# Kernel tuning notes

Hardware: AMD Instinct MI355X
Metric: run time of the kernel (lower is better)

Reference implementation:

```python
import jax, jax.numpy as jnp
import numpy as np

D_MODEL, D_STATE, D_CONV, D_INNER = 768, 16, 4, 1536
B, L = 4, 4096


def setup_inputs() -> dict:
    key = jax.random.key(0)
    ks = jax.random.split(key, 9)
    s = 0.02
    return {
        "x": jax.random.normal(ks[0], (B, L, D_MODEL), jnp.float32),
        "w_in": jax.random.normal(ks[1], (2 * D_INNER, D_MODEL), jnp.float32) * s,
        "w_conv": jax.random.normal(ks[2], (D_INNER, 1, D_CONV), jnp.float32) * 0.2,
        "w_xproj": jax.random.normal(ks[3], (2 * D_STATE + 1, D_INNER), jnp.float32) * s,
        "w_dt": jax.random.normal(ks[4], (D_INNER, 1), jnp.float32) * s,
        "b_dt": jax.random.normal(ks[5], (D_INNER,), jnp.float32) * 0.1,
        "a_log": jnp.log(jnp.tile(jnp.arange(1, D_STATE + 1, dtype=jnp.float32), (D_INNER, 1))),
        "d_param": jnp.ones((D_INNER,), jnp.float32),
        "w_out": jax.random.normal(ks[6], (D_MODEL, D_INNER), jnp.float32) * s,
    }


def _mamba_fwd(x, w_in, w_conv, w_xproj, w_dt, b_dt, a_log, d_param, w_out):
    Lseq = x.shape[1]
    xz = x @ w_in.T                                  # [B,L,2*Di]
    xs, z = jnp.split(xz, 2, axis=-1)                # [B,L,Di] each
    # depthwise causal conv1d (padding=d_conv-1, then crop to L == left-pad causal)
    xc = xs.transpose(0, 2, 1)                       # [B,Di,L]
    xc = jax.lax.conv_general_dilated(
        xc, w_conv, window_strides=(1,), padding=[(D_CONV - 1, 0)],
        feature_group_count=D_INNER, dimension_numbers=("NCH", "OIH", "NCH"))
    xs = jax.nn.silu(xc.transpose(0, 2, 1))          # [B,L,Di]
    # selective SSM parameters
    proj = xs @ w_xproj.T                            # [B,L,1+2N]
    delta_raw = proj[..., :1]                        # [B,L,1]
    b_proj = proj[..., 1:1 + D_STATE]                # [B,L,N]
    c_proj = proj[..., 1 + D_STATE:]                 # [B,L,N]
    delta = jax.nn.softplus(delta_raw @ w_dt.T + b_dt)   # [B,L,Di]
    a_mat = -jnp.exp(a_log)                          # [Di,N]

    def step(h, inp):
        dt, bt, ct, xt = inp                         # [B,Di],[B,N],[B,N],[B,Di]
        a_bar = jnp.exp(dt[:, :, None] * a_mat)      # [B,Di,N]
        h = a_bar * h + dt[:, :, None] * bt[:, None, :] * xt[:, :, None]
        y = jnp.einsum("bn,bdn->bd", ct, h) + d_param * xt
        return h, y

    h0 = jnp.zeros((x.shape[0], D_INNER, D_STATE), x.dtype)
    # time-major inputs for scan
    inputs = (delta.transpose(1, 0, 2), b_proj.transpose(1, 0, 2),
              c_proj.transpose(1, 0, 2), xs.transpose(1, 0, 2))
    _, ys = jax.lax.scan(step, h0, inputs, length=Lseq)
    y = ys.transpose(1, 0, 2)                        # [B,L,Di]
    return (y * jax.nn.silu(z)) @ w_out.T            # [B,L,d_model]


def reference(x, w_in, w_conv, w_xproj, w_dt, b_dt, a_log, d_param, w_out):
    return _mamba_fwd(x, w_in, w_conv, w_xproj, w_dt, b_dt, a_log, d_param, w_out)
```

## Files before the change

### kernel.cpp

```cpp
#include <hip/hip_runtime.h>
#include <hip/hip_bf16.h>

#define D_MODEL 768
#define D_STATE 16
#define D_INNER 1536
#define BB 4
#define LL 4096

typedef __bf16 bf16_t;
typedef __bf16 bf16x8 __attribute__((ext_vector_type(8)));
typedef __bf16 bf16x4 __attribute__((ext_vector_type(4)));
typedef float f32x4 __attribute__((ext_vector_type(4)));

__global__ __launch_bounds__(256) void cvt_all(
    const float4* __restrict__ x4, bf16x4* __restrict__ xb4,
    const float* __restrict__ w_in, const float* __restrict__ w_out,
    const float* __restrict__ w_xproj, bf16_t* __restrict__ wibf,
    bf16_t* __restrict__ wobf, bf16_t* __restrict__ wxpbf) {
  int i = blockIdx.x * 256 + threadIdx.x;
  float4 v = x4[i];
  bf16x4 o;
  o[0] = (bf16_t)v.x; o[1] = (bf16_t)v.y; o[2] = (bf16_t)v.z; o[3] = (bf16_t)v.w;
  xb4[i] = o;
  if (i < 1179648) {
    wibf[i] = (bf16_t)w_in[i];
    wibf[i + 1179648] = (bf16_t)w_in[i + 1179648];
    wobf[i] = (bf16_t)w_out[i];
    if (i < 196608) {
      int row = i / 1536;
      wxpbf[i] = (row < 33) ? (bf16_t)w_xproj[i] : (bf16_t)0.f;
    }
  }
}

template <typename CT, bool ATOMIC, bool GATE>
__global__ __launch_bounds__(256, 4) void gemm_bf16_mfma(
    const bf16_t* __restrict__ A, const bf16_t* __restrict__ B,
    CT* __restrict__ C, int K, int Klen, int ldc, int ncols) {
  __shared__ __align__(16) bf16_t As[128 * 32];
  __shared__ __align__(16) bf16_t Bs[128 * 32];
  const int t = threadIdx.x;
  const int lane = t & 63;
  const int wid = t >> 6;
  const int wm = (wid >> 1) * 64;
  const int wn = (wid & 1) * 64;
  const long Nbase = (long)blockIdx.x * 128;
  const long Mbase = (long)blockIdx.y * 128;
  const long koff = (long)blockIdx.z * Klen;

  const int r0 = t >> 2;
  const int c0 = (((t & 3) ^ ((t >> 2) & 3))) * 8;

  const bf16_t* ap0 = A + (Mbase + r0) * K + koff + c0;
  const bf16_t* ap1 = ap0 + 64 * (long)K;
  const bf16_t* bp0 = B + (Nbase + r0) * K + koff + c0;
  const bf16_t* bp1 = bp0 + 64 * (long)K;

  f32x4 acc[4][4];
#pragma unroll
  for (int i = 0; i < 4; ++i)
#pragma unroll
    for (int j = 0; j < 4; ++j) acc[i][j] = (f32x4){0.f, 0.f, 0.f, 0.f};

  const int lrow = lane & 15;
  const int lchunk = ((lane >> 4) ^ (lrow & 3)) * 8;

  for (int k0 = 0; k0 < Klen; k0 += 32) {
    if (k0) __syncthreads();
    __builtin_amdgcn_global_load_lds(
        (const __attribute__((address_space(1))) unsigned int*)ap0,
        (__attribute__((address_space(3))) unsigned int*)(&As[t * 8]), 16, 0, 0);
    __builtin_amdgcn_global_load_lds(
        (const __attribute__((address_space(1))) unsigned int*)ap1,
        (__attribute__((address_space(3))) unsigned int*)(&As[(256 + t) * 8]), 16, 0, 0);
    __builtin_amdgcn_global_load_lds(
        (const __attribute__((address_space(1))) unsigned int*)bp0,
        (__attribute__((address_space(3))) unsigned int*)(&Bs[t * 8]), 16, 0, 0);
    __builtin_amdgcn_global_load_lds(
        (const __attribute__((address_space(1))) unsigned int*)bp1,
        (__attribute__((address_space(3))) unsigned int*)(&Bs[(256 + t) * 8]), 16, 0, 0);
    ap0 += 32; ap1 += 32; bp0 += 32; bp1 += 32;
    __syncthreads();

    bf16x8 af[4], bfr[4];
#pragma unroll
    for (int i = 0; i < 4; ++i)
      af[i] = *(const bf16x8*)(&As[(wm + i * 16 + lrow) * 32 + lchunk]);
#pragma unroll
    for (int j = 0; j < 4; ++j)
      bfr[j] = *(const bf16x8*)(&Bs[(wn + j * 16 + lrow) * 32 + lchunk]);
#pragma unroll
    for (int i = 0; i < 4; ++i)
#pragma unroll
      for (int j = 0; j < 4; ++j)
        acc[i][j] = __builtin_amdgcn_mfma_f32_16x16x32_bf16(af[i], bfr[j], acc[i][j], 0, 0, 0);
  }

  const int orow = (lane >> 4) * 4;
  const int ocol = lane & 15;
#pragma unroll
  for (int i = 0; i < 4; ++i) {
#pragma unroll
    for (int j = 0; j < 4; ++j) {
      int col = (int)Nbase + wn + j * 16 + ocol;
      if (col < ncols) {
        long rowb = Mbase + wm + i * 16 + orow;
#pragma unroll
        for (int r = 0; r < 4; ++r) {
          float v = acc[i][j][r];
          if (ATOMIC) {
            atomicAdd((float*)&C[(rowb + r) * (long)ldc + col], v);
          } else {
            if (GATE && col >= 1536) v = v / (1.f + __expf(-v));
            C[(rowb + r) * (long)ldc + col] = (CT)v;
          }
        }
      }
    }
  }
}

__global__ __launch_bounds__(256) void conv_silu(const bf16_t* __restrict__ xz,
                                                 const float4* __restrict__ wconv,
                                                 bf16_t* __restrict__ xc) {
  long T = (long)blockIdx.x * 256 + threadIdx.x;
  int d = (int)(T % 1536);
  long r = T / 1536;
  int l0 = (int)(r & 511) * 8;
  long b = r >> 9;
  float4 w = wconv[d];
  const bf16_t* xs = xz + ((long)b * LL + l0) * 3072 + d;
  float v[11];
  if (l0 == 0) {
    v[0] = 0.f; v[1] = 0.f; v[2] = 0.f;
  } else {
    v[0] = (float)xs[-3 * 3072]; v[1] = (float)xs[-2 * 3072]; v[2] = (float)xs[-3072];
  }
#pragma unroll
  for (int j = 3; j < 11; ++j) v[j] = (float)xs[(j - 3) * 3072];
  bf16_t* o = xc + ((long)b * LL + l0) * 1536 + d;
#pragma unroll
  for (int i = 0; i < 8; ++i) {
    float acc = w.x * v[i];
    acc = fmaf(w.y, v[i + 1], acc);
    acc = fmaf(w.z, v[i + 2], acc);
    acc = fmaf(w.w, v[i + 3], acc);
    o[(long)i * 1536] = (bf16_t)(acc / (1.f + __expf(-acc)));
  }
}

__device__ __forceinline__ float softplus_f(float x) {
  return (x > 15.f) ? x : __logf(1.f + __expf(x));
}


__global__ __launch_bounds__(256) void scan_p1(
    const bf16_t* __restrict__ xc, const float* __restrict__ proj,
    const float* __restrict__ w_dt, const float* __restrict__ b_dt,
    float4* __restrict__ hend, float* __restrict__ Ssum) {
  __shared__ __align__(16) float prs_bc[64 * 32];
  __shared__ float prs_d[64];
  const int c = blockIdx.x;
  const int b = blockIdx.z;
  const int t = threadIdx.x;
  const int d = blockIdx.y * 256 + t;
  const long blbase = (long)b * LL + (long)c * 64;

  const float* src = proj + blbase * 33;
  for (int i = t; i < 2112; i += 256) {
    int row = i / 33, col = i - row * 33;
    float v = src[i];
    if (col == 0) prs_d[row] = v; else prs_bc[row * 32 + col - 1] = v;
  }
  __syncthreads();

  const float wdt = w_dt[d];
  const float bdt = b_dt[d];
  float h[16];
#pragma unroll
  for (int n = 0; n < 16; ++n) h[n] = 0.f;
  float S = 0.f;

  for (int l = 0; l < 64; ++l) {
    float delta = softplus_f(fmaf(prs_d[l], wdt, bdt));
    S += delta;
    float E = __expf(-delta);
    float xt = (float)xc[(blbase + l) * 1536 + d];
    float dx = delta * xt;
    const f32x4* bc = (const f32x4*)&prs_bc[l * 32];
    float ab = E;
#pragma unroll
    for (int q = 0; q < 4; ++q) {
      f32x4 Bq = bc[q];
#pragma unroll
      for (int k = 0; k < 4; ++k) {
        h[q * 4 + k] = fmaf(ab, h[q * 4 + k], dx * Bq[k]);
        ab *= E;
      }
    }
  }
  long ob = ((long)b * 64 + c) * 1536 + d;
#pragma unroll
  for (int q = 0; q < 4; ++q)
    hend[ob * 4 + q] = (float4){h[q * 4], h[q * 4 + 1], h[q * 4 + 2], h[q * 4 + 3]};
  Ssum[ob] = S;
}

__global__ __launch_bounds__(256) void scan_p2(float* __restrict__ hend,
                                               const float* __restrict__ Ssum,
                                               const float* __restrict__ a_log) {
  int idx = blockIdx.x * 256 + threadIdx.x;
  int n = idx & 15;
  int dn = idx >> 4;
  int d = dn % 1536;
  int b = dn / 1536;
  float a = -__expf(a_log[d * 16 + n]);
  float hs = 0.f;
  for (int c = 0; c < 64; ++c) {
    long ob = ((long)b * 64 + c) * 1536 + d;
    float e = hend[ob * 16 + n];
    float S = Ssum[ob];
    hend[ob * 16 + n] = hs;
    hs = fmaf(__expf(a * S), hs, e);
  }
}

__global__ __launch_bounds__(256) void scan_p3(
    const bf16_t* __restrict__ xc, const float* __restrict__ proj,
    const bf16_t* __restrict__ xz, const float* __restrict__ w_dt,
    const float* __restrict__ b_dt, const float* __restrict__ d_param,
    const float4* __restrict__ hstart, bf16_t* __restrict__ ymul) {
  __shared__ __align__(16) float prs_bc[64 * 32];
  __shared__ float prs_d[64];
  const int c = blockIdx.x;
  const int b = blockIdx.z;
  const int t = threadIdx.x;
  const int d = blockIdx.y * 256 + t;
  const long blbase = (long)b * LL + (long)c * 64;

  const float* src = proj + blbase * 33;
  for (int i = t; i < 2112; i += 256) {
    int row = i / 33, col = i - row * 33;
    float v = src[i];
    if (col == 0) prs_d[row] = v; else prs_bc[row * 32 + col - 1] = v;
  }
  __syncthreads();

  const float wdt = w_dt[d];
  const float bdt = b_dt[d];
  const float Dv = d_param[d];
  long ob = ((long)b * 64 + c) * 1536 + d;
  float h[16];
#pragma unroll
  for (int q = 0; q < 4; ++q) {
    float4 h4 = hstart[ob * 4 + q];
    h[q * 4] = h4.x; h[q * 4 + 1] = h4.y; h[q * 4 + 2] = h4.z; h[q * 4 + 3] = h4.w;
  }

  for (int l = 0; l < 64; ++l) {
    float delta = softplus_f(fmaf(prs_d[l], wdt, bdt));
    float E = __expf(-delta);
    float xt = (float)xc[(blbase + l) * 1536 + d];
    float dx = delta * xt;
    const f32x4* bc = (const f32x4*)&prs_bc[l * 32];
    float ab = E;
    float y = 0.f;
#pragma unroll
    for (int q = 0; q < 4; ++q) {
      f32x4 Bq = bc[q];
      f32x4 Cq = bc[q + 4];
#pragma unroll
      for (int k = 0; k < 4; ++k) {
        h[q * 4 + k] = fmaf(ab, h[q * 4 + k], dx * Bq[k]);
        y = fmaf(Cq[k], h[q * 4 + k], y);
        ab *= E;
      }
    }
    y = fmaf(Dv, xt, y);
    float gz = (float)xz[(blbase + l) * 3072 + 1536 + d];
    ymul[(blbase + l) * 1536 + d] = (bf16_t)(y * gz);
  }
}

extern "C" void kernel_launch(void* const* d_in, const int* in_sizes, int n_in,
                              void* d_out, int out_size, void* d_ws, size_t ws_size,
                              hipStream_t stream) {
  const float* x       = (const float*)d_in[0];
  const float* w_in    = (const float*)d_in[1];
  const float* w_conv  = (const float*)d_in[2];
  const float* w_xproj = (const float*)d_in[3];
  const float* w_dt    = (const float*)d_in[4];
  const float* b_dt    = (const float*)d_in[5];
  const float* a_log   = (const float*)d_in[6];
  const float* d_param = (const float*)d_in[7];
  const float* w_out   = (const float*)d_in[8];
  float* out = (float*)d_out;

  char* ws = (char*)d_ws;
  bf16_t* xz    = (bf16_t*)ws;  ws += 100663296;
  bf16_t* xc    = (bf16_t*)ws;  ws += 50331648;
  float*  proj  = (float*)ws;   ws += 2162688;
  float*  hend  = (float*)ws;   ws += 25165824;
  float*  Ssum  = (float*)ws;   ws += 1572864;
  bf16_t* wobf  = (bf16_t*)ws;  ws += 2359296;
  bf16_t* wxpbf = (bf16_t*)ws;  ws += 393216;
  bf16_t* ymul  = (bf16_t*)ws;  ws += 50331648;
  bf16_t* xbf   = ymul;
  bf16_t* wibf  = ymul + 12582912;

  cvt_all<<<12288, 256, 0, stream>>>((const float4*)x, (bf16x4*)xbf,
                                     w_in, w_out, w_xproj, wibf, wobf, wxpbf);

  gemm_bf16_mfma<bf16_t, false, true><<<dim3(24, 128, 1), 256, 0, stream>>>(
      xbf, wibf, xz, 768, 768, 3072, 3072);

  conv_silu<<<12288, 256, 0, stream>>>(xz, (const float4*)w_conv, xc);

  hipMemsetAsync(proj, 0, 2162688, stream);
  gemm_bf16_mfma<float, true, false><<<dim3(1, 128, 4), 256, 0, stream>>>(
      xc, wxpbf, proj, 1536, 384, 33, 33);

  scan_p1<<<dim3(64, 6, 4), 256, 0, stream>>>(xc, proj, w_dt, b_dt,
                                              (float4*)hend, Ssum);
  scan_p2<<<384, 256, 0, stream>>>(hend, Ssum, a_log);
  scan_p3<<<dim3(64, 6, 4), 256, 0, stream>>>(xc, proj, xz, w_dt, b_dt, d_param,
                                              (const float4*)hend, ymul);

  gemm_bf16_mfma<float, false, false><<<dim3(6, 128, 1), 256, 0, stream>>>(
      ymul, wobf, out, 1536, 1536, 768, 768);
}
```

Before: 466.6 us.

## Use BK=64 GEMM tiles and a dedicated narrow x_proj GEMM kernel

The main in/out GEMMs now stage 64-wide K tiles, which halves the number of barrier-separated iterations, and the grid mapping is swapped so M varies fastest. The old XOR LDS swizzle is dropped, which may bring back LDS bank conflicts. x_proj gets its own kernel with 256-row M tiles against a 64-column padded B, split-K of 8, and atomic accumulation. This stops the kernel from wasting compute on a 128-wide N tile when only 33 columns are needed, and the padded weight buffer shrinks to 64 rows.

```diff
diff --git a/kernel.cpp b/kernel.cpp
--- a/kernel.cpp
+++ b/kernel.cpp
@@ -11,6 +11,9 @@
 typedef __bf16 bf16x8 __attribute__((ext_vector_type(8)));
 typedef __bf16 bf16x4 __attribute__((ext_vector_type(4)));
 typedef float f32x4 __attribute__((ext_vector_type(4)));
+
+#define AS1 __attribute__((address_space(1)))
+#define AS3 __attribute__((address_space(3)))
 
 __global__ __launch_bounds__(256) void cvt_all(
     const float4* __restrict__ x4, bf16x4* __restrict__ xb4,
@@ -26,35 +29,37 @@
     wibf[i] = (bf16_t)w_in[i];
     wibf[i + 1179648] = (bf16_t)w_in[i + 1179648];
     wobf[i] = (bf16_t)w_out[i];
-    if (i < 196608) {
+    if (i < 98304) {
       int row = i / 1536;
       wxpbf[i] = (row < 33) ? (bf16_t)w_xproj[i] : (bf16_t)0.f;
     }
   }
 }
 
-template <typename CT, bool ATOMIC, bool GATE>
-__global__ __launch_bounds__(256, 4) void gemm_bf16_mfma(
+template <typename CT, bool GATE>
+__global__ __launch_bounds__(256, 4) void gemm_bk64(
     const bf16_t* __restrict__ A, const bf16_t* __restrict__ B,
-    CT* __restrict__ C, int K, int Klen, int ldc, int ncols) {
-  __shared__ __align__(16) bf16_t As[128 * 32];
-  __shared__ __align__(16) bf16_t Bs[128 * 32];
+    CT* __restrict__ C, int K, int ldc, int ncols) {
+  __shared__ __align__(16) bf16_t As[128 * 64];
+  __shared__ __align__(16) bf16_t Bs[128 * 64];
   const int t = threadIdx.x;
   const int lane = t & 63;
   const int wid = t >> 6;
   const int wm = (wid >> 1) * 64;
   const int wn = (wid & 1) * 64;
-  const long Nbase = (long)blockIdx.x * 128;
-  const long Mbase = (long)blockIdx.y * 128;
-  const long koff = (long)blockIdx.z * Klen;
-
-  const int r0 = t >> 2;
-  const int c0 = (((t & 3) ^ ((t >> 2) & 3))) * 8;
-
-  const bf16_t* ap0 = A + (Mbase + r0) * K + koff + c0;
-  const bf16_t* ap1 = ap0 + 64 * (long)K;
-  const bf16_t* bp0 = B + (Nbase + r0) * K + koff + c0;
-  const bf16_t* bp1 = bp0 + 64 * (long)K;
+  const long Mbase = (long)blockIdx.x * 128;
+  const long Nbase = (long)blockIdx.y * 128;
+
+  const int sr = t >> 3;
+  const int sc = (t & 7) * 8;
+
+  const bf16_t* ap[4];
+  const bf16_t* bp[4];
+#pragma unroll
+  for (int h = 0; h < 4; ++h) {
+    ap[h] = A + (Mbase + h * 32 + sr) * K + sc;
+    bp[h] = B + (Nbase + h * 32 + sr) * K + sc;
+  }
 
   f32x4 acc[4][4];
 #pragma unroll
@@ -63,37 +68,41 @@
     for (int j = 0; j < 4; ++j) acc[i][j] = (f32x4){0.f, 0.f, 0.f, 0.f};
 
   const int lrow = lane & 15;
-  const int lchunk = ((lane >> 4) ^ (lrow & 3)) * 8;
-
-  for (int k0 = 0; k0 < Klen; k0 += 32) {
+  const int lk = (lane >> 4) * 8;
+
+  for (int k0 = 0; k0 < K; k0 += 64) {
     if (k0) __syncthreads();
-    __builtin_amdgcn_global_load_lds(
-        (const __attribute__((address_space(1))) unsigned int*)ap0,
-        (__attribute__((address_space(3))) unsigned int*)(&As[t * 8]), 16, 0, 0);
-    __builtin_amdgcn_global_load_lds(
-        (const __attribute__((address_space(1))) unsigned int*)ap1,
-        (__attribute__((address_space(3))) unsigned int*)(&As[(256 + t) * 8]), 16, 0, 0);
-    __builtin_amdgcn_global_load_lds(
-        (const __attribute__((address_space(1))) unsigned int*)bp0,
-        (__attribute__((address_space(3))) unsigned int*)(&Bs[t * 8]), 16, 0, 0);
-    __builtin_amdgcn_global_load_lds(
-        (const __attribute__((address_space(1))) unsigned int*)bp1,
-        (__attribute__((address_space(3))) unsigned int*)(&Bs[(256 + t) * 8]), 16, 0, 0);
-    ap0 += 32; ap1 += 32; bp0 += 32; bp1 += 32;
+#pragma unroll
+    for (int h = 0; h < 4; ++h) {
+      __builtin_amdgcn_global_load_lds(
+          (const AS1 unsigned int*)ap[h],
+          (AS3 unsigned int*)(&As[(h * 256 + t) * 8]), 16, 0, 0);
+      ap[h] += 64;
+    }
+#pragma unroll
+    for (int h = 0; h < 4; ++h) {
+      __builtin_amdgcn_global_load_lds(
+          (const AS1 unsigned int*)bp[h],
+          (AS3 unsigned int*)(&Bs[(h * 256 + t) * 8]), 16, 0, 0);
+      bp[h] += 64;
+    }
     __syncthreads();
 
-    bf16x8 af[4], bfr[4];
-#pragma unroll
-    for (int i = 0; i < 4; ++i)
-      af[i] = *(const bf16x8*)(&As[(wm + i * 16 + lrow) * 32 + lchunk]);
-#pragma unroll
-    for (int j = 0; j < 4; ++j)
-      bfr[j] = *(const bf16x8*)(&Bs[(wn + j * 16 + lrow) * 32 + lchunk]);
-#pragma unroll
-    for (int i = 0; i < 4; ++i)
+#pragma unroll
+    for (int s = 0; s < 2; ++s) {
+      bf16x8 af[4], bfr[4];
+#pragma unroll
+      for (int i = 0; i < 4; ++i)
+        af[i] = *(const bf16x8*)(&As[(wm + i * 16 + lrow) * 64 + s * 32 + lk]);
 #pragma unroll
       for (int j = 0; j < 4; ++j)
-        acc[i][j] = __builtin_amdgcn_mfma_f32_16x16x32_bf16(af[i], bfr[j], acc[i][j], 0, 0, 0);
+        bfr[j] = *(const bf16x8*)(&Bs[(wn + j * 16 + lrow) * 64 + s * 32 + lk]);
+#pragma unroll
+      for (int i = 0; i < 4; ++i)
+#pragma unroll
+        for (int j = 0; j < 4; ++j)
+          acc[i][j] = __builtin_amdgcn_mfma_f32_16x16x32_bf16(af[i], bfr[j], acc[i][j], 0, 0, 0);
+    }
   }
 
   const int orow = (lane >> 4) * 4;
@@ -108,13 +117,83 @@
 #pragma unroll
         for (int r = 0; r < 4; ++r) {
           float v = acc[i][j][r];
-          if (ATOMIC) {
-            atomicAdd((float*)&C[(rowb + r) * (long)ldc + col], v);
-          } else {
-            if (GATE && col >= 1536) v = v / (1.f + __expf(-v));
-            C[(rowb + r) * (long)ldc + col] = (CT)v;
-          }
+          if (GATE && col >= 1536) v = v / (1.f + __expf(-v));
+          C[(rowb + r) * (long)ldc + col] = (CT)v;
         }
+      }
+    }
+  }
+}
+
+__global__ __launch_bounds__(256, 4) void gemm_xproj(
+    const bf16_t* __restrict__ A, const bf16_t* __restrict__ B,
+    float* __restrict__ C, int K, int Klen) {
+  __shared__ __align__(16) bf16_t As[256 * 32];
+  __shared__ __align__(16) bf16_t Bs[64 * 32];
+  const int t = threadIdx.x;
+  const int lane = t & 63;
+  const int wid = t >> 6;
+  const int wm = wid * 64;
+  const long Mbase = (long)blockIdx.x * 256;
+  const long koff = (long)blockIdx.z * Klen;
+
+  const int sr = t >> 2;
+  const int sc = (t & 3) * 8;
+
+  const bf16_t* ap[4];
+#pragma unroll
+  for (int h = 0; h < 4; ++h) ap[h] = A + (Mbase + h * 64 + sr) * K + koff + sc;
+  const bf16_t* bp = B + (long)sr * K + koff + sc;
+
+  f32x4 acc[4][4];
+#pragma unroll
+  for (int i = 0; i < 4; ++i)
+#pragma unroll
+    for (int j = 0; j < 4; ++j) acc[i][j] = (f32x4){0.f, 0.f, 0.f, 0.f};
+
+  const int lrow = lane & 15;
+  const int lk = (lane >> 4) * 8;
+
+  for (int k0 = 0; k0 < Klen; k0 += 32) {
+    if (k0) __syncthreads();
+#pragma unroll
+    for (int h = 0; h < 4; ++h) {
+      __builtin_amdgcn_global_load_lds(
+          (const AS1 unsigned int*)ap[h],
+          (AS3 unsigned int*)(&As[(h * 256 + t) * 8]), 16, 0, 0);
+      ap[h] += 32;
+    }
+    __builtin_amdgcn_global_load_lds(
+        (const AS1 unsigned int*)bp,
+        (AS3 unsigned int*)(&Bs[t * 8]), 16, 0, 0);
+    bp += 32;
+    __syncthreads();
+
+    bf16x8 bfr[4];
+#pragma unroll
+    for (int j = 0; j < 4; ++j)
+      bfr[j] = *(const bf16x8*)(&Bs[(j * 16 + lrow) * 32 + lk]);
+#pragma unroll
+    for (int i = 0; i < 4; ++i) {
+      bf16x8 af = *(const bf16x8*)(&As[(wm + i * 16 + lrow) * 32 + lk]);
+#pragma unroll
+      for (int j = 0; j < 4; ++j)
+        acc[i][j] = __builtin_amdgcn_mfma_f32_16x16x32_bf16(af, bfr[j], acc[i][j], 0, 0, 0);
+    }
+  }
+
+  const int orow = (lane >> 4) * 4;
+  const int ocol = lane & 15;
+#pragma unroll
+  for (int i = 0; i < 4; ++i) {
+    long rowb = Mbase + wm + i * 16 + orow;
+#pragma unroll
+    for (int j = 0; j < 3; ++j) {
+      int col = j * 16 + ocol;
+      if (col < 33) {
+#pragma unroll
+        for (int r = 0; r < 4; ++r)
+          atomicAdd(&C[(rowb + r) * 33L + col], acc[i][j][r]);
       }
     }
   }
@@ -303,7 +382,7 @@
   float*  hend  = (float*)ws;   ws += 25165824;
   float*  Ssum  = (float*)ws;   ws += 1572864;
   bf16_t* wobf  = (bf16_t*)ws;  ws += 2359296;
-  bf16_t* wxpbf = (bf16_t*)ws;  ws += 393216;
+  bf16_t* wxpbf = (bf16_t*)ws;  ws += 196608;
   bf16_t* ymul  = (bf16_t*)ws;  ws += 50331648;
   bf16_t* xbf   = ymul;
   bf16_t* wibf  = ymul + 12582912;
@@ -311,14 +390,13 @@
   cvt_all<<<12288, 256, 0, stream>>>((const float4*)x, (bf16x4*)xbf,
                                      w_in, w_out, w_xproj, wibf, wobf, wxpbf);
 
-  gemm_bf16_mfma<bf16_t, false, true><<<dim3(24, 128, 1), 256, 0, stream>>>(
-      xbf, wibf, xz, 768, 768, 3072, 3072);
+  gemm_bk64<bf16_t, true><<<dim3(128, 24), 256, 0, stream>>>(
+      xbf, wibf, xz, 768, 3072, 3072);
 
   conv_silu<<<12288, 256, 0, stream>>>(xz, (const float4*)w_conv, xc);
 
   hipMemsetAsync(proj, 0, 2162688, stream);
-  gemm_bf16_mfma<float, true, false><<<dim3(1, 128, 4), 256, 0, stream>>>(
-      xc, wxpbf, proj, 1536, 384, 33, 33);
+  gemm_xproj<<<dim3(64, 1, 8), 256, 0, stream>>>(xc, wxpbf, proj, 1536, 192);
 
   scan_p1<<<dim3(64, 6, 4), 256, 0, stream>>>(xc, proj, w_dt, b_dt,
                                               (float4*)hend, Ssum);
@@ -326,6 +404,6 @@
   scan_p3<<<dim3(64, 6, 4), 256, 0, stream>>>(xc, proj, xz, w_dt, b_dt, d_param,
                                               (const float4*)hend, ymul);
 
-  gemm_bf16_mfma<float, false, false><<<dim3(6, 128, 1), 256, 0, stream>>>(
-      ymul, wobf, out, 1536, 1536, 768, 768);
-}
+  gemm_bk64<float, false><<<dim3(128, 6), 256, 0, stream>>>(
+      ymul, wobf, out, 1536, 768, 768);
+}
```

New measurement: 466.0 us. No clear change (-0.1%).
